# Optimization experiments

Measured on AMD Instinct MI355X. Metric: run time of the kernel, lower is better.

The kernel has to match this reference:

```python
import jax, jax.numpy as jnp
import numpy as np

EPS = 1e-6

def setup_inputs() -> dict:
    key = jax.random.key(0)
    k1, k2, k3 = jax.random.split(key, 3)
    B, N, D, K = 8, 4096, 512, 8
    x = jax.random.normal(k1, (B, N, D), dtype=jnp.float32)
    W = jax.random.normal(k2, (D, K), dtype=jnp.float32) * (1.0 / np.sqrt(D))
    b = jnp.zeros((K,), dtype=jnp.float32)
    eps = jax.random.normal(k3, (B, K, D), dtype=jnp.float32)
    return {"x": x, "W": W, "b": b, "eps": eps}

def reference(x, W, b, eps):
    # x: [B,N,D], W: [D,K], b: [K], eps: [B,K,D]
    logits = jnp.einsum('bnd,dk->bnk', x, W) + b          # [B,N,K]
    probs = jax.nn.softmax(logits, axis=-1)               # softmax over clusters
    p = jnp.swapaxes(probs, 1, 2)                         # [B,K,N]
    # weighted sums (NOT normalized over N, matching the original)
    mu_k = jnp.einsum('bkn,bnd->bkd', p, x)               # [B,K,D]
    diff = x[:, None, :, :] - mu_k[:, :, None, :]         # [B,K,N,D]
    sigma_k = jnp.einsum('bkn,bknd->bkd', p, diff * diff) # [B,K,D]
    z_k = mu_k + eps * jnp.sqrt(sigma_k + EPS)            # reparameterization
    kl = -0.5 * jnp.sum(1.0 + jnp.log(sigma_k + EPS) - mu_k * mu_k - sigma_k, axis=-1)  # [B,K]
    kl_loss = jnp.mean(kl)
    pooled_z = jnp.mean(z_k, axis=1)                      # [B,D]
    return pooled_z, kl_loss
```

## Files before the change

### kernel.cpp

```cpp
#include <hip/hip_runtime.h>


typedef float v2f __attribute__((ext_vector_type(2)));

#define B_ 8
#define N_ 4096
#define D_ 512
#define K_ 8
#define EPS_ 1e-6f
#define CHUNKS 32
#define WAVES 8
#define ROWS_PER_WAVE 16

#define P_FLOATS ((size_t)B_ * N_ * K_)

__global__ __launch_bounds__(512, 2)
void kA_probs(const float* __restrict__ x, const float* __restrict__ W,
              const float* __restrict__ bias, float* __restrict__ P,
              float* __restrict__ s0p, int cstride, int atomic_mode) {
#pragma clang fp contract(fast)
  const int lane = threadIdx.x & 63;
  const int wave = threadIdx.x >> 6;
  const int b    = blockIdx.x >> 5;
  const int chunk= blockIdx.x & 31;
  const int m    = lane & 7;
  const int grp  = lane >> 3;
  const int d0   = lane * 4;

  v2f wk[8][4];
#pragma unroll
  for (int c = 0; c < 4; ++c) {
    const float4* wr0 = reinterpret_cast<const float4*>(&W[(d0 + c) * K_]);
    float4 wa = wr0[0], wb = wr0[1];
    wk[c][0] = (v2f){wa.x, wa.y}; wk[c][1] = (v2f){wa.z, wa.w};
    wk[c][2] = (v2f){wb.x, wb.y}; wk[c][3] = (v2f){wb.z, wb.w};
    const float4* wr1 = reinterpret_cast<const float4*>(&W[(256 + d0 + c) * K_]);
    float4 wc = wr1[0], wd = wr1[1];
    wk[4+c][0] = (v2f){wc.x, wc.y}; wk[4+c][1] = (v2f){wc.z, wc.w};
    wk[4+c][2] = (v2f){wd.x, wd.y}; wk[4+c][3] = (v2f){wd.z, wd.w};
  }
  const float biasv = bias[m];

  const bool c0 = (lane & 1) != 0;
  const bool c1 = (lane & 2) != 0;
  const bool c2 = (lane & 4) != 0;

  const int row_base = chunk * (WAVES * ROWS_PER_WAVE) + wave * ROWS_PER_WAVE;
  const float* xb = x + (size_t)b * N_ * D_;
  float* Pb = P + ((size_t)b * N_ + row_base) * K_;

  float s0acc = 0.f;

  for (int batch = 0; batch < 2; ++batch) {
    float psel = 0.f;
#pragma unroll
    for (int j = 0; j < 8; ++j) {
      const int row = row_base + batch * 8 + j;
      const float4* xr = reinterpret_cast<const float4*>(&xb[(size_t)row * D_]);
      float4 xa = xr[lane];
      float4 xc = xr[64 + lane];
      float xv[8] = {xa.x, xa.y, xa.z, xa.w, xc.x, xc.y, xc.z, xc.w};

      v2f qp[4] = {(v2f){0,0},(v2f){0,0},(v2f){0,0},(v2f){0,0}};
#pragma unroll
      for (int dj = 0; dj < 8; ++dj) {
        v2f xx = (v2f){xv[dj], xv[dj]};
#pragma unroll
        for (int kp = 0; kp < 4; ++kp) qp[kp] += wk[dj][kp] * xx;
      }
      float q0=qp[0].x,q1=qp[0].y,q2=qp[1].x,q3=qp[1].y;
      float q4=qp[2].x,q5=qp[2].y,q6=qp[3].x,q7=qp[3].y;

      float r0 = c0 ? q0 : q1, r1 = c0 ? q2 : q3, r2 = c0 ? q4 : q5, r3 = c0 ? q6 : q7;
      r0 = __shfl_xor(r0, 1, 64); r1 = __shfl_xor(r1, 1, 64);
      r2 = __shfl_xor(r2, 1, 64); r3 = __shfl_xor(r3, 1, 64);
      float a0 = (c0 ? q1 : q0) + r0, a1 = (c0 ? q3 : q2) + r1;
      float a2 = (c0 ? q5 : q4) + r2, a3 = (c0 ? q7 : q6) + r3;
      float s0g = c1 ? a0 : a1, s1g = c1 ? a2 : a3;
      s0g = __shfl_xor(s0g, 2, 64); s1g = __shfl_xor(s1g, 2, 64);
      float b0 = (c1 ? a1 : a0) + s0g, b1 = (c1 ? a3 : a2) + s1g;
      float g0 = c2 ? b0 : b1;
      g0 = __shfl_xor(g0, 4, 64);
      float t = (c2 ? b1 : b0) + g0;
      t += __shfl_xor(t, 8, 64);
      t += __shfl_xor(t, 16, 64);
      t += __shfl_xor(t, 32, 64);
      t += biasv;

      float mx = fmaxf(t, __shfl_xor(t, 1, 64));
      mx = fmaxf(mx, __shfl_xor(mx, 2, 64));
      mx = fmaxf(mx, __shfl_xor(mx, 4, 64));
      float e = __expf(t - mx);
      float se = e + __shfl_xor(e, 1, 64);
      se += __shfl_xor(se, 2, 64);
      se += __shfl_xor(se, 4, 64);
      float pm = e * __builtin_amdgcn_rcpf(se);

      s0acc += pm;
      psel = (grp == j) ? pm : psel;
    }
    Pb[batch * 64 + lane] = psel;
  }

  __shared__ float s0sh[WAVES][K_];
  if (lane < K_) s0sh[wave][lane] = s0acc;
  __syncthreads();
  if (threadIdx.x < K_) {
    float s = 0.f;
#pragma unroll
    for (int w = 0; w < WAVES; ++w) s += s0sh[w][threadIdx.x];
    const int cslot = atomic_mode ? 0 : chunk;
    float* dst = s0p + (size_t)(b * cstride + cslot) * K_ + threadIdx.x;
    if (atomic_mode) atomicAdd(dst, s); else *dst = s;
  }
}

__global__ __launch_bounds__(512, 2)
void kB_moments(const float* __restrict__ x, const float* __restrict__ P,
                float* __restrict__ partial, int cstride, int atomic_mode) {
#pragma clang fp contract(fast)
  const int lane = threadIdx.x & 63;
  const int wave = threadIdx.x >> 6;
  const int b    = blockIdx.x >> 5;
  const int chunk= blockIdx.x & 31;

  v2f acc[8][8];
#pragma unroll
  for (int dj = 0; dj < 8; ++dj)
#pragma unroll
    for (int k = 0; k < 8; ++k) acc[dj][k] = (v2f){0.f, 0.f};

  const int row_base = chunk * (WAVES * ROWS_PER_WAVE) + wave * ROWS_PER_WAVE;
  const float* xb = x + (size_t)b * N_ * D_;
  const float* Prow = P + ((size_t)b * N_ + row_base) * K_;

  const float4* xr = reinterpret_cast<const float4*>(&xb[(size_t)row_base * D_]);
  float4 xa = xr[lane];
  float4 xc = xr[64 + lane];
  const float4* pr = reinterpret_cast<const float4*>(Prow);
  float4 pA = pr[0], pB = pr[1];

  for (int i = 0; i < ROWS_PER_WAVE; ++i) {
    const int ni = (i + 1 < ROWS_PER_WAVE) ? i + 1 : i;
    const float4* xrn = reinterpret_cast<const float4*>(&xb[(size_t)(row_base + ni) * D_]);
    float4 na = xrn[lane];
    float4 nc = xrn[64 + lane];
    const float4* prn = reinterpret_cast<const float4*>(Prow + (size_t)ni * K_);
    float4 npA = prn[0], npB = prn[1];

    float xv[8] = {xa.x, xa.y, xa.z, xa.w, xc.x, xc.y, xc.z, xc.w};
    float pk[8] = {pA.x, pA.y, pA.z, pA.w, pB.x, pB.y, pB.z, pB.w};

#pragma unroll
    for (int dj = 0; dj < 8; ++dj) {
      v2f m2 = (v2f){xv[dj], xv[dj] * xv[dj]};
#pragma unroll
      for (int k = 0; k < 8; ++k) {
        v2f pp = (v2f){pk[k], pk[k]};
        acc[dj][k] += m2 * pp;
      }
    }

    xa = na; xc = nc; pA = npA; pB = npB;
  }

  const int cslot = atomic_mode ? 0 : chunk;
  __shared__ v2f sh[WAVES][2][K_][64];

#pragma unroll
  for (int r = 0; r < 4; ++r) {
#pragma unroll
    for (int k = 0; k < 8; ++k) {
      sh[wave][0][k][lane] = acc[2*r][k];
      sh[wave][1][k][lane] = acc[2*r + 1][k];
    }
    __syncthreads();
    v2f sA = sh[0][0][wave][lane];
    v2f sB = sh[0][1][wave][lane];
#pragma unroll
    for (int w = 1; w < WAVES; ++w) {
      sA += sh[w][0][wave][lane];
      sB += sh[w][1][wave][lane];
    }
    const int d = (r < 2) ? (lane * 4 + 2 * r) : (256 + lane * 4 + (2 * r - 4));
    float* dst = partial + (((size_t)(b * cstride + cslot) * K_ + wave) * D_ + d) * 2;
    if (atomic_mode) {
      atomicAdd(dst + 0, sA.x); atomicAdd(dst + 1, sA.y);
      atomicAdd(dst + 2, sB.x); atomicAdd(dst + 3, sB.y);
    } else {
      float4 v; v.x = sA.x; v.y = sA.y; v.z = sB.x; v.w = sB.y;
      *reinterpret_cast<float4*>(dst) = v;
    }
    __syncthreads();
  }
}

__global__ __launch_bounds__(128)
void k2_final(const float* __restrict__ partial, const float* __restrict__ s0p,
              const float* __restrict__ eps, float* __restrict__ out,
              int cstride, int nchunks) {
  const int b = blockIdx.x >> 5;
  const int slice = blockIdx.x & 31;
  const int tid = threadIdx.x;
  const int k = tid >> 4;
  const int dl = tid & 15;
  const int d = slice * 16 + dl;

  __shared__ float s0sh[K_];
  __shared__ float zsh[K_][16];
  __shared__ float klsh[2];

  if (tid < K_) {
    float s = 0.f;
    for (int c = 0; c < nchunks; ++c) s += s0p[(size_t)(b * cstride + c) * K_ + tid];
    s0sh[tid] = s;
  }
  __syncthreads();

  float S1 = 0.f, S2 = 0.f;
  for (int c = 0; c < nchunks; ++c) {
    const v2f v = *reinterpret_cast<const v2f*>(
        partial + (((size_t)(b * cstride + c) * K_ + k) * D_ + d) * 2);
    S1 += v.x; S2 += v.y;
  }
  const float S0 = s0sh[k];
  float sigraw = S2 + (S0 - 2.f) * S1 * S1;
  float sig = fmaxf(sigraw, 0.f) + EPS_;
  float z = S1 + eps[((size_t)(b * K_ + k)) * D_ + d] * sqrtf(sig);
  zsh[k][dl] = z;
  float klp = 1.f + logf(sig) - S1 * S1 - sigraw;

  klp += __shfl_xor(klp, 1, 64);
  klp += __shfl_xor(klp, 2, 64);
  klp += __shfl_xor(klp, 4, 64);
  klp += __shfl_xor(klp, 8, 64);
  klp += __shfl_xor(klp, 16, 64);
  klp += __shfl_xor(klp, 32, 64);
  const int lane = tid & 63, wv = tid >> 6;
  if (lane == 0) klsh[wv] = klp;
  __syncthreads();

  if (tid < 16) {
    float pooled = 0.f;
#pragma unroll
    for (int kk = 0; kk < K_; ++kk) pooled += zsh[kk][tid];
    out[b * D_ + slice * 16 + tid] = pooled * 0.125f;
  }
  if (tid == 0) {
    atomicAdd(out + B_ * D_, (klsh[0] + klsh[1]) * (-0.5f / (B_ * K_)));
  }
}

extern "C" void kernel_launch(void* const* d_in, const int* in_sizes, int n_in,
                              void* d_out, int out_size, void* d_ws, size_t ws_size,
                              hipStream_t stream) {
  const float* x    = (const float*)d_in[0];
  const float* W    = (const float*)d_in[1];
  const float* bias = (const float*)d_in[2];
  const float* eps  = (const float*)d_in[3];
  float* out = (float*)d_out;
  float* ws  = (float*)d_ws;

  const size_t full_floats =
      P_FLOATS + (size_t)B_ * CHUNKS * K_ * D_ * 2 + (size_t)B_ * CHUNKS * K_;
  const int atomic_mode = (ws_size < full_floats * sizeof(float)) ? 1 : 0;
  const int cstride = atomic_mode ? 1 : CHUNKS;
  const int nchunks = atomic_mode ? 1 : CHUNKS;

  float* P       = ws;
  float* partial = ws + P_FLOATS;
  float* s0p     = partial + (size_t)B_ * cstride * K_ * D_ * 2;

  if (atomic_mode) {
    const size_t zbytes =
        ((size_t)B_ * K_ * D_ * 2 + (size_t)B_ * K_) * sizeof(float);
    hipMemsetAsync(partial, 0, zbytes, stream);
  }
  hipMemsetAsync(out + B_ * D_, 0, sizeof(float), stream);

  kA_probs  <<<B_ * CHUNKS, 64 * WAVES, 0, stream>>>(x, W, bias, P, s0p, cstride, atomic_mode);
  kB_moments<<<B_ * CHUNKS, 64 * WAVES, 0, stream>>>(x, P, partial, cstride, atomic_mode);
  k2_final  <<<B_ * 32, 128, 0, stream>>>(partial, s0p, eps, out, cstride, nchunks);
}
```

Before: 61.25 us.

## Split work into more smaller blocks and partition clusters across waves

Raises the chunk count from 32 to 128 and shrinks blocks to 256 threads, so each GPU kernel launches four times as many blocks. The moments kernel now gives each wave pair half of the clusters over the same 16 rows, which halves accumulator registers and allows higher occupancy. The cluster-mass sums now go through a global atomic instead of per-chunk slots. The final kernel splits its chunk reduction across two thread halves. The trade-off is a four-times-larger partial buffer written and read through memory, plus duplicate x reads by paired waves.

```diff
diff --git a/kernel.cpp b/kernel.cpp
--- a/kernel.cpp
+++ b/kernel.cpp
@@ -8,21 +8,19 @@
 #define D_ 512
 #define K_ 8
 #define EPS_ 1e-6f
-#define CHUNKS 32
-#define WAVES 8
-#define ROWS_PER_WAVE 16
-
+#define CHUNKS 128
 #define P_FLOATS ((size_t)B_ * N_ * K_)
-
-__global__ __launch_bounds__(512, 2)
+#define PART_FLOATS(cs) ((size_t)B_ * (cs) * K_ * D_ * 2)
+
+__global__ __launch_bounds__(256, 3)
 void kA_probs(const float* __restrict__ x, const float* __restrict__ W,
               const float* __restrict__ bias, float* __restrict__ P,
-              float* __restrict__ s0p, int cstride, int atomic_mode) {
+              float* __restrict__ s0g) {
 #pragma clang fp contract(fast)
   const int lane = threadIdx.x & 63;
   const int wave = threadIdx.x >> 6;
-  const int b    = blockIdx.x >> 5;
-  const int chunk= blockIdx.x & 31;
+  const int b    = blockIdx.x >> 7;
+  const int chunk= blockIdx.x & 127;
   const int m    = lane & 7;
   const int grp  = lane >> 3;
   const int d0   = lane * 4;
@@ -41,194 +39,203 @@
   }
   const float biasv = bias[m];
 
-  const bool c0 = (lane & 1) != 0;
-  const bool c1 = (lane & 2) != 0;
-  const bool c2 = (lane & 4) != 0;
-
-  const int row_base = chunk * (WAVES * ROWS_PER_WAVE) + wave * ROWS_PER_WAVE;
+  const bool s_c0 = (lane & 1) != 0;
+  const bool s_c1 = (lane & 2) != 0;
+  const bool s_c2 = (lane & 4) != 0;
+
+  const int wrow = chunk * 32 + wave * 8;
   const float* xb = x + (size_t)b * N_ * D_;
-  float* Pb = P + ((size_t)b * N_ + row_base) * K_;
+
+  auto row_softmax = [&](float4 xa, float4 xc) -> float {
+    float xv[8] = {xa.x, xa.y, xa.z, xa.w, xc.x, xc.y, xc.z, xc.w};
+    v2f qp[4] = {(v2f){0,0},(v2f){0,0},(v2f){0,0},(v2f){0,0}};
+#pragma unroll
+    for (int dj = 0; dj < 8; ++dj) {
+      v2f xx = (v2f){xv[dj], xv[dj]};
+#pragma unroll
+      for (int kp = 0; kp < 4; ++kp) qp[kp] += wk[dj][kp] * xx;
+    }
+    float q0=qp[0].x,q1=qp[0].y,q2=qp[1].x,q3=qp[1].y;
+    float q4=qp[2].x,q5=qp[2].y,q6=qp[3].x,q7=qp[3].y;
+    float r0 = s_c0 ? q0 : q1, r1 = s_c0 ? q2 : q3, r2 = s_c0 ? q4 : q5, r3 = s_c0 ? q6 : q7;
+    r0 = __shfl_xor(r0, 1, 64); r1 = __shfl_xor(r1, 1, 64);
+    r2 = __shfl_xor(r2, 1, 64); r3 = __shfl_xor(r3, 1, 64);
+    float a0 = (s_c0 ? q1 : q0) + r0, a1 = (s_c0 ? q3 : q2) + r1;
+    float a2 = (s_c0 ? q5 : q4) + r2, a3 = (s_c0 ? q7 : q6) + r3;
+    float s0g_ = s_c1 ? a0 : a1, s1g_ = s_c1 ? a2 : a3;
+    s0g_ = __shfl_xor(s0g_, 2, 64); s1g_ = __shfl_xor(s1g_, 2, 64);
+    float b0 = (s_c1 ? a1 : a0) + s0g_, b1 = (s_c1 ? a3 : a2) + s1g_;
+    float g0 = s_c2 ? b0 : b1;
+    g0 = __shfl_xor(g0, 4, 64);
+    float t = (s_c2 ? b1 : b0) + g0;
+    t += __shfl_xor(t, 8, 64);
+    t += __shfl_xor(t, 16, 64);
+    t += __shfl_xor(t, 32, 64);
+    t += biasv;
+    float mx = fmaxf(t, __shfl_xor(t, 1, 64));
+    mx = fmaxf(mx, __shfl_xor(mx, 2, 64));
+    mx = fmaxf(mx, __shfl_xor(mx, 4, 64));
+    float e = __expf(t - mx);
+    float se = e + __shfl_xor(e, 1, 64);
+    se += __shfl_xor(se, 2, 64);
+    se += __shfl_xor(se, 4, 64);
+    return e * __builtin_amdgcn_rcpf(se);
+  };
 
   float s0acc = 0.f;
-
-  for (int batch = 0; batch < 2; ++batch) {
-    float psel = 0.f;
-#pragma unroll
-    for (int j = 0; j < 8; ++j) {
-      const int row = row_base + batch * 8 + j;
-      const float4* xr = reinterpret_cast<const float4*>(&xb[(size_t)row * D_]);
-      float4 xa = xr[lane];
-      float4 xc = xr[64 + lane];
-      float xv[8] = {xa.x, xa.y, xa.z, xa.w, xc.x, xc.y, xc.z, xc.w};
-
-      v2f qp[4] = {(v2f){0,0},(v2f){0,0},(v2f){0,0},(v2f){0,0}};
-#pragma unroll
-      for (int dj = 0; dj < 8; ++dj) {
-        v2f xx = (v2f){xv[dj], xv[dj]};
-#pragma unroll
-        for (int kp = 0; kp < 4; ++kp) qp[kp] += wk[dj][kp] * xx;
-      }
-      float q0=qp[0].x,q1=qp[0].y,q2=qp[1].x,q3=qp[1].y;
-      float q4=qp[2].x,q5=qp[2].y,q6=qp[3].x,q7=qp[3].y;
-
-      float r0 = c0 ? q0 : q1, r1 = c0 ? q2 : q3, r2 = c0 ? q4 : q5, r3 = c0 ? q6 : q7;
-      r0 = __shfl_xor(r0, 1, 64); r1 = __shfl_xor(r1, 1, 64);
-      r2 = __shfl_xor(r2, 1, 64); r3 = __shfl_xor(r3, 1, 64);
-      float a0 = (c0 ? q1 : q0) + r0, a1 = (c0 ? q3 : q2) + r1;
-      float a2 = (c0 ? q5 : q4) + r2, a3 = (c0 ? q7 : q6) + r3;
-      float s0g = c1 ? a0 : a1, s1g = c1 ? a2 : a3;
-      s0g = __shfl_xor(s0g, 2, 64); s1g = __shfl_xor(s1g, 2, 64);
-      float b0 = (c1 ? a1 : a0) + s0g, b1 = (c1 ? a3 : a2) + s1g;
-      float g0 = c2 ? b0 : b1;
-      g0 = __shfl_xor(g0, 4, 64);
-      float t = (c2 ? b1 : b0) + g0;
-      t += __shfl_xor(t, 8, 64);
-      t += __shfl_xor(t, 16, 64);
-      t += __shfl_xor(t, 32, 64);
-      t += biasv;
-
-      float mx = fmaxf(t, __shfl_xor(t, 1, 64));
-      mx = fmaxf(mx, __shfl_xor(mx, 2, 64));
-      mx = fmaxf(mx, __shfl_xor(mx, 4, 64));
-      float e = __expf(t - mx);
-      float se = e + __shfl_xor(e, 1, 64);
-      se += __shfl_xor(se, 2, 64);
-      se += __shfl_xor(se, 4, 64);
-      float pm = e * __builtin_amdgcn_rcpf(se);
-
-      s0acc += pm;
-      psel = (grp == j) ? pm : psel;
-    }
-    Pb[batch * 64 + lane] = psel;
-  }
-
-  __shared__ float s0sh[WAVES][K_];
+  float psel = 0.f;
+#pragma unroll
+  for (int pair = 0; pair < 4; ++pair) {
+    const int r0 = wrow + pair * 2;
+    const float4* x0 = reinterpret_cast<const float4*>(&xb[(size_t)r0 * D_]);
+    const float4* x1 = reinterpret_cast<const float4*>(&xb[(size_t)(r0 + 1) * D_]);
+    float4 xa0 = x0[lane], xc0 = x0[64 + lane];
+    float4 xa1 = x1[lane], xc1 = x1[64 + lane];
+    float pm0 = row_softmax(xa0, xc0);
+    float pm1 = row_softmax(xa1, xc1);
+    s0acc += pm0 + pm1;
+    psel = (grp == pair * 2)     ? pm0 : psel;
+    psel = (grp == pair * 2 + 1) ? pm1 : psel;
+  }
+  P[((size_t)b * N_ + wrow) * K_ + lane] = psel;
+
+  __shared__ float s0sh[4][K_];
   if (lane < K_) s0sh[wave][lane] = s0acc;
   __syncthreads();
   if (threadIdx.x < K_) {
-    float s = 0.f;
-#pragma unroll
-    for (int w = 0; w < WAVES; ++w) s += s0sh[w][threadIdx.x];
-    const int cslot = atomic_mode ? 0 : chunk;
-    float* dst = s0p + (size_t)(b * cstride + cslot) * K_ + threadIdx.x;
-    if (atomic_mode) atomicAdd(dst, s); else *dst = s;
-  }
-}
-
-__global__ __launch_bounds__(512, 2)
+    float s = s0sh[0][threadIdx.x] + s0sh[1][threadIdx.x] +
+              s0sh[2][threadIdx.x] + s0sh[3][threadIdx.x];
+    atomicAdd(s0g + b * K_ + threadIdx.x, s);
+  }
+}
+
+__global__ __launch_bounds__(256, 4)
 void kB_moments(const float* __restrict__ x, const float* __restrict__ P,
                 float* __restrict__ partial, int cstride, int atomic_mode) {
 #pragma clang fp contract(fast)
-  const int lane = threadIdx.x & 63;
-  const int wave = threadIdx.x >> 6;
-  const int b    = blockIdx.x >> 5;
-  const int chunk= blockIdx.x & 31;
-
-  v2f acc[8][8];
+  const int lane  = threadIdx.x & 63;
+  const int wave  = threadIdx.x >> 6;
+  const int khalf = wave & 1;
+  const int rowg  = wave >> 1;
+  const int b     = blockIdx.x >> 7;
+  const int chunk = blockIdx.x & 127;
+
+  v2f acc[8][4];
 #pragma unroll
   for (int dj = 0; dj < 8; ++dj)
 #pragma unroll
-    for (int k = 0; k < 8; ++k) acc[dj][k] = (v2f){0.f, 0.f};
-
-  const int row_base = chunk * (WAVES * ROWS_PER_WAVE) + wave * ROWS_PER_WAVE;
+    for (int kk = 0; kk < 4; ++kk) acc[dj][kk] = (v2f){0.f, 0.f};
+
+  const int row_base = chunk * 32 + rowg * 16;
   const float* xb = x + (size_t)b * N_ * D_;
-  const float* Prow = P + ((size_t)b * N_ + row_base) * K_;
+  const float* Pr = P + ((size_t)b * N_ + row_base) * K_ + khalf * 4;
 
   const float4* xr = reinterpret_cast<const float4*>(&xb[(size_t)row_base * D_]);
   float4 xa = xr[lane];
   float4 xc = xr[64 + lane];
-  const float4* pr = reinterpret_cast<const float4*>(Prow);
-  float4 pA = pr[0], pB = pr[1];
-
-  for (int i = 0; i < ROWS_PER_WAVE; ++i) {
-    const int ni = (i + 1 < ROWS_PER_WAVE) ? i + 1 : i;
+  float4 pv = *reinterpret_cast<const float4*>(Pr);
+
+  for (int i = 0; i < 16; ++i) {
+    const int ni = (i + 1 < 16) ? i + 1 : i;
     const float4* xrn = reinterpret_cast<const float4*>(&xb[(size_t)(row_base + ni) * D_]);
     float4 na = xrn[lane];
     float4 nc = xrn[64 + lane];
-    const float4* prn = reinterpret_cast<const float4*>(Prow + (size_t)ni * K_);
-    float4 npA = prn[0], npB = prn[1];
+    float4 npv = *reinterpret_cast<const float4*>(Pr + (size_t)ni * K_);
 
     float xv[8] = {xa.x, xa.y, xa.z, xa.w, xc.x, xc.y, xc.z, xc.w};
-    float pk[8] = {pA.x, pA.y, pA.z, pA.w, pB.x, pB.y, pB.z, pB.w};
+    float pk[4] = {pv.x, pv.y, pv.z, pv.w};
 
 #pragma unroll
     for (int dj = 0; dj < 8; ++dj) {
       v2f m2 = (v2f){xv[dj], xv[dj] * xv[dj]};
 #pragma unroll
-      for (int k = 0; k < 8; ++k) {
-        v2f pp = (v2f){pk[k], pk[k]};
-        acc[dj][k] += m2 * pp;
+      for (int kk = 0; kk < 4; ++kk) {
+        v2f pp = (v2f){pk[kk], pk[kk]};
+        acc[dj][kk] += m2 * pp;
       }
     }
-
-    xa = na; xc = nc; pA = npA; pB = npB;
+    xa = na; xc = nc; pv = npv;
   }
 
   const int cslot = atomic_mode ? 0 : chunk;
-  __shared__ v2f sh[WAVES][2][K_][64];
+  __shared__ v2f sh[4][2][4][64];
 
 #pragma unroll
   for (int r = 0; r < 4; ++r) {
 #pragma unroll
-    for (int k = 0; k < 8; ++k) {
-      sh[wave][0][k][lane] = acc[2*r][k];
-      sh[wave][1][k][lane] = acc[2*r + 1][k];
+    for (int kk = 0; kk < 4; ++kk) {
+      sh[wave][0][kk][lane] = acc[2 * r][kk];
+      sh[wave][1][kk][lane] = acc[2 * r + 1][kk];
     }
     __syncthreads();
-    v2f sA = sh[0][0][wave][lane];
-    v2f sB = sh[0][1][wave][lane];
-#pragma unroll
-    for (int w = 1; w < WAVES; ++w) {
-      sA += sh[w][0][wave][lane];
-      sB += sh[w][1][wave][lane];
-    }
-    const int d = (r < 2) ? (lane * 4 + 2 * r) : (256 + lane * 4 + (2 * r - 4));
-    float* dst = partial + (((size_t)(b * cstride + cslot) * K_ + wave) * D_ + d) * 2;
-    if (atomic_mode) {
-      atomicAdd(dst + 0, sA.x); atomicAdd(dst + 1, sA.y);
-      atomicAdd(dst + 2, sB.x); atomicAdd(dst + 3, sB.y);
-    } else {
-      float4 v; v.x = sA.x; v.y = sA.y; v.z = sB.x; v.w = sB.y;
-      *reinterpret_cast<float4*>(dst) = v;
+    const int k8 = threadIdx.x >> 5;
+    const int w0 = k8 >> 2;
+    const int kk = k8 & 3;
+#pragma unroll
+    for (int half = 0; half < 2; ++half) {
+      const int slot = (threadIdx.x & 31) + 32 * half;
+      v2f sA = sh[w0][0][kk][slot] + sh[w0 + 2][0][kk][slot];
+      v2f sB = sh[w0][1][kk][slot] + sh[w0 + 2][1][kk][slot];
+      const int dbase = (r < 2) ? (slot * 4 + 2 * r) : (256 + slot * 4 + 2 * (r - 2));
+      float* dst = partial + (((size_t)(b * cstride + cslot) * K_ + k8) * D_ + dbase) * 2;
+      if (atomic_mode) {
+        atomicAdd(dst + 0, sA.x); atomicAdd(dst + 1, sA.y);
+        atomicAdd(dst + 2, sB.x); atomicAdd(dst + 3, sB.y);
+      } else {
+        float4 v; v.x = sA.x; v.y = sA.y; v.z = sB.x; v.w = sB.y;
+        *reinterpret_cast<float4*>(dst) = v;
+      }
     }
     __syncthreads();
   }
 }
 
-__global__ __launch_bounds__(128)
-void k2_final(const float* __restrict__ partial, const float* __restrict__ s0p,
+__global__ __launch_bounds__(256)
+void k2_final(const float* __restrict__ partial, const float* __restrict__ s0g,
               const float* __restrict__ eps, float* __restrict__ out,
               int cstride, int nchunks) {
   const int b = blockIdx.x >> 5;
   const int slice = blockIdx.x & 31;
   const int tid = threadIdx.x;
-  const int k = tid >> 4;
+  const int cq = tid >> 7;
+  const int k  = (tid >> 4) & 7;
   const int dl = tid & 15;
-  const int d = slice * 16 + dl;
-
-  __shared__ float s0sh[K_];
+  const int d  = slice * 16 + dl;
+
+  __shared__ v2f red2[2][K_][16];
   __shared__ float zsh[K_][16];
-  __shared__ float klsh[2];
-
-  if (tid < K_) {
-    float s = 0.f;
-    for (int c = 0; c < nchunks; ++c) s += s0p[(size_t)(b * cstride + c) * K_ + tid];
-    s0sh[tid] = s;
-  }
+  __shared__ float klsh[4];
+
+  const int half = (nchunks + 1) >> 1;
+  const int cbeg = cq * half;
+  const int cend = (cbeg + half < nchunks) ? (cbeg + half) : nchunks;
+
+  const float* base = partial + (((size_t)b * cstride) * K_ + k) * D_ * 2 + d * 2;
+  const size_t cstep = (size_t)K_ * D_ * 2;
+
+  v2f s0v = (v2f){0,0}, s1v = (v2f){0,0}, s2v = (v2f){0,0}, s3v = (v2f){0,0};
+  int c = cbeg;
+  for (; c + 4 <= cend; c += 4) {
+    s0v += *reinterpret_cast<const v2f*>(base + (size_t)c * cstep);
+    s1v += *reinterpret_cast<const v2f*>(base + (size_t)(c + 1) * cstep);
+    s2v += *reinterpret_cast<const v2f*>(base + (size_t)(c + 2) * cstep);
+    s3v += *reinterpret_cast<const v2f*>(base + (size_t)(c + 3) * cstep);
+  }
+  for (; c < cend; ++c) s0v += *reinterpret_cast<const v2f*>(base + (size_t)c * cstep);
+  red2[cq][k][dl] = (s0v + s1v) + (s2v + s3v);
   __syncthreads();
 
-  float S1 = 0.f, S2 = 0.f;
-  for (int c = 0; c < nchunks; ++c) {
-    const v2f v = *reinterpret_cast<const v2f*>(
-        partial + (((size_t)(b * cstride + c) * K_ + k) * D_ + d) * 2);
-    S1 += v.x; S2 += v.y;
-  }
-  const float S0 = s0sh[k];
-  float sigraw = S2 + (S0 - 2.f) * S1 * S1;
-  float sig = fmaxf(sigraw, 0.f) + EPS_;
-  float z = S1 + eps[((size_t)(b * K_ + k)) * D_ + d] * sqrtf(sig);
-  zsh[k][dl] = z;
-  float klp = 1.f + logf(sig) - S1 * S1 - sigraw;
+  float klp = 0.f;
+  if (cq == 0) {
+    v2f sv = red2[0][k][dl] + red2[1][k][dl];
+    const float S1 = sv.x, S2 = sv.y;
+    const float S0 = s0g[b * K_ + k];
+    float sigraw = S2 + (S0 - 2.f) * S1 * S1;
+    float sig = fmaxf(sigraw, 0.f) + EPS_;
+    float z = S1 + eps[((size_t)(b * K_ + k)) * D_ + d] * sqrtf(sig);
+    zsh[k][dl] = z;
+    klp = 1.f + logf(sig) - S1 * S1 - sigraw;
+  }
 
   klp += __shfl_xor(klp, 1, 64);
   klp += __shfl_xor(klp, 2, 64);
@@ -247,7 +254,7 @@
     out[b * D_ + slice * 16 + tid] = pooled * 0.125f;
   }
   if (tid == 0) {
-    atomicAdd(out + B_ * D_, (klsh[0] + klsh[1]) * (-0.5f / (B_ * K_)));
+    atomicAdd(out + B_ * D_, (klsh[0] + klsh[1] + klsh[2] + klsh[3]) * (-0.5f / (B_ * K_)));
   }
 }
 
@@ -261,24 +268,23 @@
   float* out = (float*)d_out;
   float* ws  = (float*)d_ws;
 
-  const size_t full_floats =
-      P_FLOATS + (size_t)B_ * CHUNKS * K_ * D_ * 2 + (size_t)B_ * CHUNKS * K_;
+  const size_t full_floats = P_FLOATS + PART_FLOATS(CHUNKS) + B_ * K_;
   const int atomic_mode = (ws_size < full_floats * sizeof(float)) ? 1 : 0;
   const int cstride = atomic_mode ? 1 : CHUNKS;
   const int nchunks = atomic_mode ? 1 : CHUNKS;
 
   float* P       = ws;
   float* partial = ws + P_FLOATS;
-  float* s0p     = partial + (size_t)B_ * cstride * K_ * D_ * 2;
+  float* s0g     = partial + PART_FLOATS(cstride);
 
   if (atomic_mode) {
-    const size_t zbytes =
-        ((size_t)B_ * K_ * D_ * 2 + (size_t)B_ * K_) * sizeof(float);
-    hipMemsetAsync(partial, 0, zbytes, stream);
+    hipMemsetAsync(partial, 0, (PART_FLOATS(1) + B_ * K_) * sizeof(float), stream);
+  } else {
+    hipMemsetAsync(s0g, 0, B_ * K_ * sizeof(float), stream);
   }
   hipMemsetAsync(out + B_ * D_, 0, sizeof(float), stream);
 
-  kA_probs  <<<B_ * CHUNKS, 64 * WAVES, 0, stream>>>(x, W, bias, P, s0p, cstride, atomic_mode);
-  kB_moments<<<B_ * CHUNKS, 64 * WAVES, 0, stream>>>(x, P, partial, cstride, atomic_mode);
-  k2_final  <<<B_ * 32, 128, 0, stream>>>(partial, s0p, eps, out, cstride, nchunks);
-}
+  kA_probs  <<<B_ * CHUNKS, 256, 0, stream>>>(x, W, bias, P, s0g);
+  kB_moments<<<B_ * CHUNKS, 256, 0, stream>>>(x, P, partial, cstride, atomic_mode);
+  k2_final  <<<B_ * 32, 256, 0, stream>>>(partial, s0g, eps, out, cstride, nchunks);
+}
```

New measurement: 236.9 us. 3.87x slower.
